# Kernel optimization log

Measured on AMD Instinct MI355X. Metric: run time of the kernel, lower is better.

The kernel has to match this reference:

```python
import jax, jax.numpy as jnp
import numpy as np

N_NODES = 50000
N_EDGES = 800000
D_IN = 64
D_ID = 32
D_H = 192
D_MSG = 64
D_UP = 128


def _mlp(x, W1, b1, W2, b2):
    # 2-layer MLP: Linear -> ReLU -> Linear (bn=False)
    return jax.nn.relu(x @ W1 + b1) @ W2 + b2


def setup_inputs() -> dict:
    key = jax.random.key(0)
    ks = jax.random.split(key, 16)
    msg_in = 2 * (D_IN + D_ID)   # 192
    upd_in = D_IN + D_MSG        # 128
    s = lambda d: 1.0 / np.sqrt(d)
    return {
        "x": jax.random.normal(ks[0], (N_NODES, D_IN), dtype=jnp.float32),
        "edge_index": jax.random.randint(ks[1], (2, N_EDGES), 0, N_NODES, dtype=jnp.int64),
        "node_centrality": jax.random.uniform(ks[2], (N_NODES,), dtype=jnp.float32),
        "edge_centrality": jax.random.uniform(ks[3], (N_EDGES,), dtype=jnp.float32),
        "identifiers": jax.random.normal(ks[4], (N_NODES, D_ID), dtype=jnp.float32),
        "degrees": jax.random.uniform(ks[5], (N_NODES, 1), dtype=jnp.float32),
        "msg_W1": jax.random.normal(ks[6], (msg_in, D_H), dtype=jnp.float32) * s(msg_in),
        "msg_b1": jnp.zeros((D_H,), dtype=jnp.float32),
        "msg_W2": jax.random.normal(ks[7], (D_H, D_MSG), dtype=jnp.float32) * s(D_H),
        "msg_b2": jnp.zeros((D_MSG,), dtype=jnp.float32),
        "upd_W1": jax.random.normal(ks[8], (upd_in, D_H), dtype=jnp.float32) * s(upd_in),
        "upd_b1": jnp.zeros((D_H,), dtype=jnp.float32),
        "upd_W2": jax.random.normal(ks[9], (D_H, D_UP), dtype=jnp.float32) * s(D_H),
        "upd_b2": jnp.zeros((D_UP,), dtype=jnp.float32),
    }


def reference(x, edge_index, node_centrality, edge_centrality, identifiers, degrees,
              msg_W1, msg_b1, msg_W2, msg_b2, upd_W1, upd_b1, upd_W2, upd_b2):
    n_nodes = x.shape[0]
    # flow='source_to_target' => select=1: i = edge_index[1] (target), j = edge_index[0]
    idx_j = edge_index[0]
    idx_i = edge_index[1]
    x_i, x_j = x[idx_i], x[idx_j]                       # [E, d_in]
    id_i, id_j = identifiers[idx_i], identifiers[idx_j]  # [E, d_id]
    msg_in = jnp.concatenate([x_i, x_j, id_i, id_j], axis=-1)  # [E, 2*(d_in+d_id)]
    msgs = _mlp(msg_in, msg_W1, msg_b1, msg_W2, msg_b2)        # [E, d_msg]
    msgs = msgs * edge_centrality[:, None]
    # torch.sparse.sum over dim 0 of COO([edge_index[0], edge_index[1]]) == segment_sum by edge_index[1]
    agg = jax.ops.segment_sum(msgs, idx_i, num_segments=n_nodes)  # [N, d_msg]
    upd_in = jnp.concatenate([x * node_centrality[:, None], agg], axis=-1)  # [N, d_in+d_msg]
    return _mlp(upd_in, upd_W1, upd_b1, upd_W2, upd_b2)  # [N, d_up]
```

## Files before the change

### kernel.cpp

```cpp
#include <hip/hip_runtime.h>
#include <hip/hip_bf16.h>

#define N_NODES 50000
#define N_EDGES 800000
#define NPAD    50048

typedef __attribute__((ext_vector_type(8))) short short8;
typedef __attribute__((ext_vector_type(4))) float f32x4;

static __device__ inline short f2bf(float f) {
    union { __hip_bfloat16 b; short s; } c; c.b = __float2bfloat16(f); return c.s;
}
static __device__ inline float bf2f(short s) {
    union { unsigned u; float f; } c; c.u = ((unsigned)(unsigned short)s) << 16; return c.f;
}
static __device__ inline float bflo(unsigned u) {
    union { unsigned v; float f; } c; c.v = u << 16; return c.f;
}
static __device__ inline float bfhi(unsigned u) {
    union { unsigned v; float f; } c; c.v = u & 0xffff0000u; return c.f;
}

__global__ __launch_bounds__(256) void k_pack(const float* __restrict__ x,
                                              const float* __restrict__ ids,
                                              const float* __restrict__ mW1,
                                              const float* __restrict__ mW2,
                                              const float* __restrict__ uW1,
                                              const float* __restrict__ uW2,
                                              __hip_bfloat16* __restrict__ Xid,
                                              __hip_bfloat16* __restrict__ W1pk,
                                              __hip_bfloat16* __restrict__ W2pk,
                                              __hip_bfloat16* __restrict__ uW1pk,
                                              __hip_bfloat16* __restrict__ uW2pk) {
    const int tid = blockIdx.x * 256 + threadIdx.x;
    const int XN = NPAD * 96 / 8;
    if (tid < XN) {
        const int n = tid / 12, c0 = (tid % 12) * 8;
        short8 v;
#pragma unroll
        for (int i = 0; i < 8; ++i) {
            const int c = c0 + i;
            float f = 0.f;
            if (n < N_NODES) f = (c < 64) ? x[n * 64 + c] : ids[n * 32 + (c - 64)];
            v[i] = f2bf(f);
        }
        *(short8*)&Xid[n * 96 + c0] = v;
        return;
    }
    int r = tid - XN;
    if (r < 3 * 24 * 64) {
        const int kt = r / (24 * 64), nt = (r / 64) % 24, l = r % 64;
        const int e = l & 15, kg = l >> 4;
        short8 v;
#pragma unroll
        for (int i = 0; i < 8; ++i) {
            const int k = kt * 32 + kg * 8 + i;
            const int col = nt * 16 + e;
            float val;
            if (col < 192) { const int row = (k < 64) ? k : k + 64;  val = mW1[row * 192 + col]; }
            else           { const int row = (k < 64) ? k + 64 : k + 96; val = mW1[row * 192 + (col - 192)]; }
            v[i] = f2bf(val);
        }
        *(short8*)&W1pk[r * 8] = v;
        return;
    }
    r -= 3 * 24 * 64;
    if (r < 6 * 4 * 64) {
        const int kt = r / (4 * 64), nt = (r / 64) % 4, l = r % 64;
        const int e = l & 15, kg = l >> 4;
        short8 v;
#pragma unroll
        for (int i = 0; i < 8; ++i)
            v[i] = f2bf(mW2[(kt * 32 + kg * 8 + i) * 64 + nt * 16 + e]);
        *(short8*)&W2pk[r * 8] = v;
        return;
    }
    r -= 6 * 4 * 64;
    if (r < 4 * 12 * 64) {
        const int kt = r / (12 * 64), nt = (r / 64) % 12, l = r % 64;
        const int e = l & 15, kg = l >> 4;
        short8 v;
#pragma unroll
        for (int i = 0; i < 8; ++i)
            v[i] = f2bf(uW1[(kt * 32 + kg * 8 + i) * 192 + nt * 16 + e]);
        *(short8*)&uW1pk[r * 8] = v;
        return;
    }
    r -= 4 * 12 * 64;
    if (r < 6 * 8 * 64) {
        const int kt = r / (8 * 64), nt = (r / 64) % 8, l = r % 64;
        const int e = l & 15, kg = l >> 4;
        short8 v;
#pragma unroll
        for (int i = 0; i < 8; ++i)
            v[i] = f2bf(uW2[(kt * 32 + kg * 8 + i) * 128 + nt * 16 + e]);
        *(short8*)&uW2pk[r * 8] = v;
    }
}

__global__ __launch_bounds__(256) void k_pre(const __hip_bfloat16* __restrict__ Xid,
                                             const __hip_bfloat16* __restrict__ W1pk,
                                             const float* __restrict__ b1,
                                             __hip_bfloat16* __restrict__ P1,
                                             __hip_bfloat16* __restrict__ P2) {
    const int t = threadIdx.x, w = t >> 6, l = t & 63;
    const int e = l & 15, kg = l >> 4;
    const int n0 = blockIdx.x * 64 + w * 16;

    short8 A[3];
#pragma unroll
    for (int kt = 0; kt < 3; ++kt)
        A[kt] = *(const short8*)&Xid[(n0 + e) * 96 + kt * 32 + kg * 8];

#pragma unroll
    for (int nt = 0; nt < 24; ++nt) {
        const float bv = (nt < 12) ? b1[nt * 16 + e] : 0.f;
        f32x4 acc = {bv, bv, bv, bv};
#pragma unroll
        for (int kt = 0; kt < 3; ++kt) {
            const short8 B = *(const short8*)&W1pk[((kt * 24 + nt) * 64 + l) * 8];
            acc = __builtin_amdgcn_mfma_f32_16x16x32_bf16(A[kt], B, acc, 0, 0, 0);
        }
#pragma unroll
        for (int r = 0; r < 4; ++r) {
            const int node = n0 + kg * 4 + r;
            if (node < N_NODES) {
                if (nt < 12) P1[node * 192 + nt * 16 + e] = __float2bfloat16(acc[r]);
                else         P2[node * 192 + (nt - 12) * 16 + e] = __float2bfloat16(acc[r]);
            }
        }
    }
}

__global__ __launch_bounds__(256) void k_edge(const int* __restrict__ ei,
                                              const float* __restrict__ ec,
                                              const __hip_bfloat16* __restrict__ P1,
                                              const __hip_bfloat16* __restrict__ P2,
                                              const __hip_bfloat16* __restrict__ W2pk,
                                              const float* __restrict__ b2,
                                              float* __restrict__ agg) {
    __shared__ uint4 w2s[6 * 4 * 64];
    const int t = threadIdx.x;
    for (int v = t; v < 1536; v += 256) w2s[v] = ((const uint4*)W2pk)[v];
    __syncthreads();

    const int w = t >> 6, l = t & 63;
    const int e = l & 15, kg = l >> 4;
    float b2v[4];
#pragma unroll
    for (int n = 0; n < 4; ++n) b2v[n] = b2[n * 16 + e];

    const int nGroups = N_EDGES / 16;
    const int wstride = gridDim.x * 4;

    for (int g = blockIdx.x * 4 + w; g < nGroups; g += wstride) {
        const int e0 = g * 16;
        const int jj = ei[e0 + e];
        const int ii = ei[N_EDGES + e0 + e];
        const __hip_bfloat16* r1 = P1 + (size_t)ii * 192 + kg * 8;
        const __hip_bfloat16* r2 = P2 + (size_t)jj * 192 + kg * 8;

        f32x4 acc0 = {0.f, 0.f, 0.f, 0.f};
        f32x4 acc1 = {0.f, 0.f, 0.f, 0.f};
        f32x4 acc2 = {0.f, 0.f, 0.f, 0.f};
        f32x4 acc3 = {0.f, 0.f, 0.f, 0.f};

#pragma unroll
        for (int tt = 0; tt < 6; ++tt) {
            union { uint4 q; unsigned u[4]; } A1, A2;
            A1.q = *(const uint4*)(r1 + tt * 32);
            A2.q = *(const uint4*)(r2 + tt * 32);
            short8 h;
#pragma unroll
            for (int p = 0; p < 4; ++p) {
                float s0 = bflo(A1.u[p]) + bflo(A2.u[p]);
                float s1 = bfhi(A1.u[p]) + bfhi(A2.u[p]);
                s0 = s0 > 0.f ? s0 : 0.f;
                s1 = s1 > 0.f ? s1 : 0.f;
                h[2 * p]     = f2bf(s0);
                h[2 * p + 1] = f2bf(s1);
            }
            acc0 = __builtin_amdgcn_mfma_f32_16x16x32_bf16(h, *(const short8*)&w2s[(tt * 4 + 0) * 64 + l], acc0, 0, 0, 0);
            acc1 = __builtin_amdgcn_mfma_f32_16x16x32_bf16(h, *(const short8*)&w2s[(tt * 4 + 1) * 64 + l], acc1, 0, 0, 0);
            acc2 = __builtin_amdgcn_mfma_f32_16x16x32_bf16(h, *(const short8*)&w2s[(tt * 4 + 2) * 64 + l], acc2, 0, 0, 0);
            acc3 = __builtin_amdgcn_mfma_f32_16x16x32_bf16(h, *(const short8*)&w2s[(tt * 4 + 3) * 64 + l], acc3, 0, 0, 0);
        }

        const float4 ecq = *(const float4*)(ec + e0 + kg * 4);
#pragma unroll
        for (int r = 0; r < 4; ++r) {
            const int edge = kg * 4 + r;
            const int it = __shfl(ii, edge);
            const float ecv = ((const float*)&ecq)[r];
            float v0 = (acc0[r] + b2v[0]) * ecv;
            float v1 = (acc1[r] + b2v[1]) * ecv;
            float v2 = (acc2[r] + b2v[2]) * ecv;
            float v3 = (acc3[r] + b2v[3]) * ecv;
            float* base = agg + (size_t)it * 64 + e;
            atomicAdd(base,      v0);
            atomicAdd(base + 16, v1);
            atomicAdd(base + 32, v2);
            atomicAdd(base + 48, v3);
        }
    }
}

__global__ __launch_bounds__(256) void k_upd(const __hip_bfloat16* __restrict__ Xid,
                                             const float* __restrict__ nc,
                                             const float* __restrict__ agg,
                                             const __hip_bfloat16* __restrict__ uW1pk,
                                             const float* __restrict__ ub1,
                                             const __hip_bfloat16* __restrict__ uW2pk,
                                             const float* __restrict__ ub2,
                                             float* __restrict__ out) {
    __shared__ char Hs[4][16 * 384];
    const int t = threadIdx.x, w = t >> 6, l = t & 63;
    const int e = l & 15, kg = l >> 4;
    const int n0 = blockIdx.x * 64 + w * 16;
    const int nodeA = n0 + e;

    const float ncv = nc[nodeA < N_NODES ? nodeA : N_NODES - 1];
    short8 A[4];
#pragma unroll
    for (int kt = 0; kt < 2; ++kt) {
        const short8 xa = *(const short8*)&Xid[nodeA * 96 + kt * 32 + kg * 8];
        short8 o;
#pragma unroll
        for (int i = 0; i < 8; ++i) o[i] = f2bf(bf2f(xa[i]) * ncv);
        A[kt] = o;
    }
#pragma unroll
    for (int kt = 2; kt < 4; ++kt) {
        const float* ap = agg + (size_t)nodeA * 64 + (kt - 2) * 32 + kg * 8;
        const float4 a0 = *(const float4*)ap;
        const float4 a1 = *(const float4*)(ap + 4);
        short8 o;
        o[0] = f2bf(a0.x); o[1] = f2bf(a0.y); o[2] = f2bf(a0.z); o[3] = f2bf(a0.w);
        o[4] = f2bf(a1.x); o[5] = f2bf(a1.y); o[6] = f2bf(a1.z); o[7] = f2bf(a1.w);
        A[kt] = o;
    }

#pragma unroll
    for (int nt = 0; nt < 12; ++nt) {
        const float bv = ub1[nt * 16 + e];
        f32x4 acc = {bv, bv, bv, bv};
#pragma unroll
        for (int kt = 0; kt < 4; ++kt) {
            const short8 B = *(const short8*)&uW1pk[((kt * 12 + nt) * 64 + l) * 8];
            acc = __builtin_amdgcn_mfma_f32_16x16x32_bf16(A[kt], B, acc, 0, 0, 0);
        }
#pragma unroll
        for (int r = 0; r < 4; ++r) {
            const int hr = kg * 4 + r;
            const float v = acc[r] > 0.f ? acc[r] : 0.f;
            int byte = hr * 384 + (nt * 16 + e) * 2;
            byte ^= (hr & 7) << 4;
            *(__hip_bfloat16*)(&Hs[w][0] + byte) = __float2bfloat16(v);
        }
    }

    short8 A2[6];
#pragma unroll
    for (int kt = 0; kt < 6; ++kt) {
        int byte = e * 384 + kt * 64 + kg * 16;
        byte ^= (e & 7) << 4;
        A2[kt] = *(const short8*)(&Hs[w][0] + byte);
    }
#pragma unroll
    for (int nt = 0; nt < 8; ++nt) {
        const float bv = ub2[nt * 16 + e];
        f32x4 acc = {bv, bv, bv, bv};
#pragma unroll
        for (int kt = 0; kt < 6; ++kt) {
            const short8 B = *(const short8*)&uW2pk[((kt * 8 + nt) * 64 + l) * 8];
            acc = __builtin_amdgcn_mfma_f32_16x16x32_bf16(A2[kt], B, acc, 0, 0, 0);
        }
#pragma unroll
        for (int r = 0; r < 4; ++r) {
            const int node = n0 + kg * 4 + r;
            if (node < N_NODES) out[node * 128 + nt * 16 + e] = acc[r];
        }
    }
}

extern "C" void kernel_launch(void* const* d_in, const int* in_sizes, int n_in,
                              void* d_out, int out_size, void* d_ws, size_t ws_size,
                              hipStream_t stream) {
    const float* x   = (const float*)d_in[0];
    const int*   ei  = (const int*)d_in[1];
    const float* ncv = (const float*)d_in[2];
    const float* ecv = (const float*)d_in[3];
    const float* ids = (const float*)d_in[4];
    const float* mW1 = (const float*)d_in[6];
    const float* mb1 = (const float*)d_in[7];
    const float* mW2 = (const float*)d_in[8];
    const float* mb2 = (const float*)d_in[9];
    const float* uW1 = (const float*)d_in[10];
    const float* ub1 = (const float*)d_in[11];
    const float* uW2 = (const float*)d_in[12];
    const float* ub2 = (const float*)d_in[13];
    float* out = (float*)d_out;

    char* ws = (char*)d_ws;
    __hip_bfloat16* Xid  = (__hip_bfloat16*)ws;                 ws += (size_t)NPAD * 96 * 2;
    __hip_bfloat16* P1   = (__hip_bfloat16*)ws;                 ws += (size_t)NPAD * 192 * 2;
    __hip_bfloat16* P2   = (__hip_bfloat16*)ws;                 ws += (size_t)NPAD * 192 * 2;
    float*          agg  = (float*)ws;                          ws += (size_t)NPAD * 64 * 4;
    __hip_bfloat16* W1pk = (__hip_bfloat16*)ws;                 ws += 3 * 24 * 64 * 8 * 2;
    __hip_bfloat16* W2pk = (__hip_bfloat16*)ws;                 ws += 6 * 4 * 64 * 8 * 2;
    __hip_bfloat16* uW1pk= (__hip_bfloat16*)ws;                 ws += 4 * 12 * 64 * 8 * 2;
    __hip_bfloat16* uW2pk= (__hip_bfloat16*)ws;                 ws += 6 * 8 * 64 * 8 * 2;

    hipMemsetAsync(agg, 0, (size_t)NPAD * 64 * sizeof(float), stream);
    const int packWork = NPAD * 96 / 8 + 3 * 24 * 64 + 6 * 4 * 64 + 4 * 12 * 64 + 6 * 8 * 64;
    k_pack<<<(packWork + 255) / 256, 256, 0, stream>>>(x, ids, mW1, mW2, uW1, uW2,
                                                       Xid, W1pk, W2pk, uW1pk, uW2pk);
    k_pre<<<NPAD / 64, 256, 0, stream>>>(Xid, W1pk, mb1, P1, P2);
    k_edge<<<2048, 256, 0, stream>>>(ei, ecv, P1, P2, W2pk, mb2, agg);
    k_upd<<<NPAD / 64, 256, 0, stream>>>(Xid, ncv, agg, uW1pk, ub1, uW2pk, ub2, out);
}
```

Baseline: 261.6 us.

## Counting-sort edges by target node before the edge MLP and scatter-add

Adds a degree histogram inside the pack kernel, a three-stage prefix scan and a scatter kernel. Together they reorder edge indices and edge centralities by target node on every call. The edge kernel then walks contiguous per-block ranges of sorted edges, so P1 gathers and atomic adds on agg hit the same target rows close together. It also hoists all six P1/P2 row loads ahead of the MFMA loop to overlap gather latency. The cost is four extra launches plus an extra pass over the edge arrays, with atomic increments for the histogram and scatter.

```diff
diff --git a/kernel.cpp b/kernel.cpp
--- a/kernel.cpp
+++ b/kernel.cpp
@@ -4,6 +4,7 @@
 #define N_NODES 50000
 #define N_EDGES 800000
 #define NPAD    50048
+#define NCHUNK  49
 
 typedef __attribute__((ext_vector_type(8))) short short8;
 typedef __attribute__((ext_vector_type(4))) float f32x4;
@@ -27,12 +28,16 @@
                                               const float* __restrict__ mW2,
                                               const float* __restrict__ uW1,
                                               const float* __restrict__ uW2,
+                                              const int* __restrict__ ei,
+                                              int* __restrict__ deg,
                                               __hip_bfloat16* __restrict__ Xid,
                                               __hip_bfloat16* __restrict__ W1pk,
                                               __hip_bfloat16* __restrict__ W2pk,
                                               __hip_bfloat16* __restrict__ uW1pk,
                                               __hip_bfloat16* __restrict__ uW2pk) {
     const int tid = blockIdx.x * 256 + threadIdx.x;
+    if (tid < N_EDGES) atomicAdd(&deg[ei[N_EDGES + tid]], 1);
+
     const int XN = NPAD * 96 / 8;
     if (tid < XN) {
         const int n = tid / 12, c0 = (tid % 12) * 8;
@@ -96,6 +101,63 @@
             v[i] = f2bf(uW2[(kt * 32 + kg * 8 + i) * 128 + nt * 16 + e]);
         *(short8*)&uW2pk[r * 8] = v;
     }
+}
+
+__global__ __launch_bounds__(64) void k_scan1(const int* __restrict__ deg,
+                                              int* __restrict__ bsum) {
+    const int base = blockIdx.x * 1024, l = threadIdx.x;
+    int s = 0;
+#pragma unroll
+    for (int q = 0; q < 16; ++q) {
+        const int i = base + q * 64 + l;
+        s += (i < NPAD) ? deg[i] : 0;
+    }
+#pragma unroll
+    for (int off = 32; off; off >>= 1) s += __shfl_xor(s, off);
+    if (l == 0) bsum[blockIdx.x] = s;
+}
+
+__global__ __launch_bounds__(64) void k_scan2(const int* __restrict__ bsum,
+                                              int* __restrict__ bbase) {
+    const int t = threadIdx.x;
+    if (t < NCHUNK) {
+        int s = 0;
+        for (int q = 0; q < t; ++q) s += bsum[q];
+        bbase[t] = s;
+    }
+}
+
+__global__ __launch_bounds__(1024) void k_scan3(const int* __restrict__ deg,
+                                                const int* __restrict__ bbase,
+                                                int* __restrict__ cursor) {
+    __shared__ int wtot[16];
+    const int t = threadIdx.x, w = t >> 6, lane = t & 63;
+    const int i = blockIdx.x * 1024 + t;
+    const int v0 = (i < NPAD) ? deg[i] : 0;
+    int v = v0;
+#pragma unroll
+    for (int off = 1; off < 64; off <<= 1) {
+        const int n = __shfl_up(v, off);
+        if (lane >= off) v += n;
+    }
+    if (lane == 63) wtot[w] = v;
+    __syncthreads();
+    int wbase = bbase[blockIdx.x];
+    for (int q = 0; q < w; ++q) wbase += wtot[q];
+    if (i < NPAD) cursor[i] = wbase + v - v0;
+}
+
+__global__ __launch_bounds__(256) void k_scatter(const int* __restrict__ ei,
+                                                 const float* __restrict__ ec,
+                                                 int* __restrict__ cursor,
+                                                 int2* __restrict__ sJI,
+                                                 float* __restrict__ sEC) {
+    const int e = blockIdx.x * 256 + threadIdx.x;
+    if (e >= N_EDGES) return;
+    const int i = ei[N_EDGES + e];
+    const int pos = atomicAdd(&cursor[i], 1);
+    sJI[pos] = make_int2(ei[e], i);
+    sEC[pos] = ec[e];
 }
 
 __global__ __launch_bounds__(256) void k_pre(const __hip_bfloat16* __restrict__ Xid,
@@ -132,8 +194,9 @@
     }
 }
 
-__global__ __launch_bounds__(256) void k_edge(const int* __restrict__ ei,
-                                              const float* __restrict__ ec,
+#define GPB 25
+__global__ __launch_bounds__(256) void k_edge(const int2* __restrict__ sJI,
+                                              const float* __restrict__ sEC,
                                               const __hip_bfloat16* __restrict__ P1,
                                               const __hip_bfloat16* __restrict__ P2,
                                               const __hip_bfloat16* __restrict__ W2pk,
@@ -150,15 +213,22 @@
 #pragma unroll
     for (int n = 0; n < 4; ++n) b2v[n] = b2[n * 16 + e];
 
-    const int nGroups = N_EDGES / 16;
-    const int wstride = gridDim.x * 4;
-
-    for (int g = blockIdx.x * 4 + w; g < nGroups; g += wstride) {
+    const int gEnd = blockIdx.x * GPB + GPB;
+
+    for (int g = blockIdx.x * GPB + w; g < gEnd; g += 4) {
         const int e0 = g * 16;
-        const int jj = ei[e0 + e];
-        const int ii = ei[N_EDGES + e0 + e];
+        const int2 ji = sJI[e0 + e];
+        const int jj = ji.x, ii = ji.y;
         const __hip_bfloat16* r1 = P1 + (size_t)ii * 192 + kg * 8;
         const __hip_bfloat16* r2 = P2 + (size_t)jj * 192 + kg * 8;
+        const float4 ecq = *(const float4*)(sEC + e0 + kg * 4);
+
+        union { uint4 q; unsigned u[4]; } A1[6], A2[6];
+#pragma unroll
+        for (int tt = 0; tt < 6; ++tt) {
+            A1[tt].q = *(const uint4*)(r1 + tt * 32);
+            A2[tt].q = *(const uint4*)(r2 + tt * 32);
+        }
 
         f32x4 acc0 = {0.f, 0.f, 0.f, 0.f};
         f32x4 acc1 = {0.f, 0.f, 0.f, 0.f};
@@ -167,14 +237,11 @@
 
 #pragma unroll
         for (int tt = 0; tt < 6; ++tt) {
-            union { uint4 q; unsigned u[4]; } A1, A2;
-            A1.q = *(const uint4*)(r1 + tt * 32);
-            A2.q = *(const uint4*)(r2 + tt * 32);
             short8 h;
 #pragma unroll
             for (int p = 0; p < 4; ++p) {
-                float s0 = bflo(A1.u[p]) + bflo(A2.u[p]);
-                float s1 = bfhi(A1.u[p]) + bfhi(A2.u[p]);
+                float s0 = bflo(A1[tt].u[p]) + bflo(A2[tt].u[p]);
+                float s1 = bfhi(A1[tt].u[p]) + bfhi(A2[tt].u[p]);
                 s0 = s0 > 0.f ? s0 : 0.f;
                 s1 = s1 > 0.f ? s1 : 0.f;
                 h[2 * p]     = f2bf(s0);
@@ -186,7 +253,6 @@
             acc3 = __builtin_amdgcn_mfma_f32_16x16x32_bf16(h, *(const short8*)&w2s[(tt * 4 + 3) * 64 + l], acc3, 0, 0, 0);
         }
 
-        const float4 ecq = *(const float4*)(ec + e0 + kg * 4);
 #pragma unroll
         for (int r = 0; r < 4; ++r) {
             const int edge = kg * 4 + r;
@@ -302,20 +368,32 @@
     float* out = (float*)d_out;
 
     char* ws = (char*)d_ws;
-    __hip_bfloat16* Xid  = (__hip_bfloat16*)ws;                 ws += (size_t)NPAD * 96 * 2;
-    __hip_bfloat16* P1   = (__hip_bfloat16*)ws;                 ws += (size_t)NPAD * 192 * 2;
-    __hip_bfloat16* P2   = (__hip_bfloat16*)ws;                 ws += (size_t)NPAD * 192 * 2;
-    float*          agg  = (float*)ws;                          ws += (size_t)NPAD * 64 * 4;
-    __hip_bfloat16* W1pk = (__hip_bfloat16*)ws;                 ws += 3 * 24 * 64 * 8 * 2;
-    __hip_bfloat16* W2pk = (__hip_bfloat16*)ws;                 ws += 6 * 4 * 64 * 8 * 2;
-    __hip_bfloat16* uW1pk= (__hip_bfloat16*)ws;                 ws += 4 * 12 * 64 * 8 * 2;
-    __hip_bfloat16* uW2pk= (__hip_bfloat16*)ws;                 ws += 6 * 8 * 64 * 8 * 2;
+    __hip_bfloat16* Xid  = (__hip_bfloat16*)ws;   ws += (size_t)NPAD * 96 * 2;
+    __hip_bfloat16* P1   = (__hip_bfloat16*)ws;   ws += (size_t)NPAD * 192 * 2;
+    __hip_bfloat16* P2   = (__hip_bfloat16*)ws;   ws += (size_t)NPAD * 192 * 2;
+    float*          agg  = (float*)ws;            ws += (size_t)NPAD * 64 * 4;
+    __hip_bfloat16* W1pk = (__hip_bfloat16*)ws;   ws += 3 * 24 * 64 * 8 * 2;
+    __hip_bfloat16* W2pk = (__hip_bfloat16*)ws;   ws += 6 * 4 * 64 * 8 * 2;
+    __hip_bfloat16* uW1pk= (__hip_bfloat16*)ws;   ws += 4 * 12 * 64 * 8 * 2;
+    __hip_bfloat16* uW2pk= (__hip_bfloat16*)ws;   ws += 6 * 8 * 64 * 8 * 2;
+    int*            deg  = (int*)ws;              ws += (size_t)NPAD * 4;
+    int*            cur  = (int*)ws;              ws += (size_t)NPAD * 4;
+    int*            bsum = (int*)ws;              ws += 64 * 4;
+    int*            bbas = (int*)ws;              ws += 64 * 4;
+    int2*           sJI  = (int2*)ws;             ws += (size_t)N_EDGES * 8;
+    float*          sEC  = (float*)ws;            ws += (size_t)N_EDGES * 4;
 
     hipMemsetAsync(agg, 0, (size_t)NPAD * 64 * sizeof(float), stream);
-    const int packWork = NPAD * 96 / 8 + 3 * 24 * 64 + 6 * 4 * 64 + 4 * 12 * 64 + 6 * 8 * 64;
-    k_pack<<<(packWork + 255) / 256, 256, 0, stream>>>(x, ids, mW1, mW2, uW1, uW2,
-                                                       Xid, W1pk, W2pk, uW1pk, uW2pk);
+    hipMemsetAsync(deg, 0, (size_t)NPAD * sizeof(int), stream);
+
+    const int packGrid = (N_EDGES + 255) / 256;
+    k_pack<<<packGrid, 256, 0, stream>>>(x, ids, mW1, mW2, uW1, uW2, ei, deg,
+                                         Xid, W1pk, W2pk, uW1pk, uW2pk);
+    k_scan1<<<NCHUNK, 64, 0, stream>>>(deg, bsum);
+    k_scan2<<<1, 64, 0, stream>>>(bsum, bbas);
+    k_scan3<<<NCHUNK, 1024, 0, stream>>>(deg, bbas, cur);
+    k_scatter<<<(N_EDGES + 255) / 256, 256, 0, stream>>>(ei, ecv, cur, sJI, sEC);
     k_pre<<<NPAD / 64, 256, 0, stream>>>(Xid, W1pk, mb1, P1, P2);
-    k_edge<<<2048, 256, 0, stream>>>(ei, ecv, P1, P2, W2pk, mb2, agg);
+    k_edge<<<N_EDGES / 16 / GPB, 256, 0, stream>>>(sJI, sEC, P1, P2, W2pk, mb2, agg);
     k_upd<<<NPAD / 64, 256, 0, stream>>>(Xid, ncv, agg, uW1pk, ub1, uW2pk, ub2, out);
 }
```

After: 863.2 us. 230% more time.
